# Kernel tuning notes

Measured on AMD Instinct MI355X. Metric: run time of the kernel, lower is better.

Reference implementation:

```python
import jax, jax.numpy as jnp
import numpy as np
import math
from functools import partial

B = 256
H = 256
HEADS = 4
DK = H // HEADS
NA_MAX, NP_MAX, NH_MAX = 127, 23, 11


def _counts():
    i = np.arange(B)
    ac = (64 + i % 64).astype(np.int32)   # atoms per graph, 64..127
    pc = (8 + i % 16).astype(np.int32)    # pharm fragments per graph, 8..23
    hc = (4 + i % 8).astype(np.int32)     # hyper-edges per graph, 4..11
    return ac, pc, hc


def setup_inputs() -> dict:
    key = jax.random.key(0)
    ks = jax.random.split(key, 32)
    ac, pc, hc = _counts()
    na, npm, nh = int(ac.sum()), int(pc.sum()), int(hc.sum())
    w = 1.0 / math.sqrt(H)
    inp = {
        'atom_message': jax.random.normal(ks[0], (na, H), jnp.float32),
        'pharm_message': jax.random.normal(ks[1], (npm, H), jnp.float32),
        'hyper_message': jax.random.normal(ks[2], (nh, H), jnp.float32),
        'atom_counts': jnp.asarray(ac),
        'pharm_counts': jnp.asarray(pc),
        'hyper_counts': jnp.asarray(hc),
    }
    # two MultiHeadedAttention blocks: q/k/v/out linears each (W stored as [in, out])
    names = []
    for pre in ('p2h', 'a2p'):
        for part in ('Wq', 'bq', 'Wk', 'bk', 'Wv', 'bv', 'Wo', 'bo'):
            names.append(f'{pre}_{part}')
    ki = 3
    for n in names:
        if n.split('_')[1].startswith('W'):
            inp[n] = jax.random.normal(ks[ki], (H, H), jnp.float32) * w
        else:
            inp[n] = jax.random.normal(ks[ki], (H,), jnp.float32) * 0.01
        ki += 1
    # bidirectional GRU params, torch layout: W_ih [3H, H], W_hh [3H, H], b [3H]
    for d in ('f', 'b'):
        inp[f'gru_Wih_{d}'] = jax.random.normal(ks[ki], (3 * H, H), jnp.float32) * w; ki += 1
        inp[f'gru_Whh_{d}'] = jax.random.normal(ks[ki], (3 * H, H), jnp.float32) * w; ki += 1
        inp[f'gru_bih_{d}'] = jax.random.normal(ks[ki], (3 * H,), jnp.float32) * 0.01; ki += 1
        inp[f'gru_bhh_{d}'] = jax.random.normal(ks[ki], (3 * H,), jnp.float32) * 0.01; ki += 1
    return inp


def _split_pad(msg, counts, max_n):
    # faithful vectorized version of split_batch: narrow + zero-pad per graph
    starts = jnp.concatenate([jnp.zeros((1,), jnp.int32), jnp.cumsum(counts)[:-1].astype(jnp.int32)])
    j = jnp.arange(max_n)
    valid = j[None, :] < counts[:, None]                       # [B, max_n]
    idx = jnp.where(valid, starts[:, None] + j[None, :], msg.shape[0])
    padded_src = jnp.concatenate([msg, jnp.zeros((1, msg.shape[1]), msg.dtype)], 0)
    return padded_src[idx], valid                              # [B, max_n, H]


def _mha(q, k, v, mask, Wq, bq, Wk, bk, Wv, bv, Wo, bo):
    Bq, Lq, _ = q.shape
    def proj(x, W, b):
        y = x @ W + b
        return y.reshape(x.shape[0], x.shape[1], HEADS, DK).transpose(0, 2, 1, 3)
    qh, kh, vh = proj(q, Wq, bq), proj(k, Wk, bk), proj(v, Wv, bv)
    scores = jnp.einsum('bhqd,bhkd->bhqk', qh, kh) / math.sqrt(DK)
    scores = jnp.where(mask[:, None], jnp.float32(-1e9), scores)
    p = jax.nn.softmax(scores, axis=-1)
    o = jnp.einsum('bhqk,bhkd->bhqd', p, vh)
    o = o.transpose(0, 2, 1, 3).reshape(Bq, Lq, H)
    return o @ Wo + bo


def _gru_dir(x, h0, Wih, Whh, bih, bhh):
    # x: [B, T, H], torch GRU cell equations
    def step(h, xt):
        gi = xt @ Wih.T + bih
        gh = h @ Whh.T + bhh
        ir, iz, inn = jnp.split(gi, 3, axis=-1)
        hr, hz, hn = jnp.split(gh, 3, axis=-1)
        r = jax.nn.sigmoid(ir + hr)
        z = jax.nn.sigmoid(iz + hz)
        n = jnp.tanh(inn + r * hn)
        h = (1.0 - z) * n + z * h
        return h, h
    _, ys = jax.lax.scan(step, h0, x.transpose(1, 0, 2))
    return ys.transpose(1, 0, 2)


def reference(atom_message, pharm_message, hyper_message,
              p2h_Wq, p2h_bq, p2h_Wk, p2h_bk, p2h_Wv, p2h_bv, p2h_Wo, p2h_bo,
              a2p_Wq, a2p_bq, a2p_Wk, a2p_bk, a2p_Wv, a2p_bv, a2p_Wo, a2p_bo,
              gru_Wih_f, gru_Whh_f, gru_bih_f, gru_bhh_f,
              gru_Wih_b, gru_Whh_b, gru_bih_b, gru_bhh_b,
              atom_counts, pharm_counts, hyper_counts):
    atom_f, atom_valid = _split_pad(atom_message, atom_counts, NA_MAX)
    pharm_f, _ = _split_pad(pharm_message, pharm_counts, NP_MAX)
    hyper_f, _ = _split_pad(hyper_message, hyper_counts, NH_MAX)

    nz = lambda t: (t != 0).astype(jnp.float32)
    mask1 = jnp.einsum('bqh,bkh->bqk', nz(pharm_f), nz(hyper_f)) == 0  # [B, Np, Nh]
    mask2 = jnp.einsum('bqh,bkh->bqk', nz(atom_f), nz(pharm_f)) == 0   # [B, Na, Np]

    pharm_f = _mha(pharm_f, hyper_f, hyper_f, mask1,
                   p2h_Wq, p2h_bq, p2h_Wk, p2h_bk, p2h_Wv, p2h_bv, p2h_Wo, p2h_bo) + pharm_f
    h = _mha(atom_f, pharm_f, pharm_f, mask2,
             a2p_Wq, a2p_bq, a2p_Wk, a2p_bk, a2p_Wv, a2p_bv, a2p_Wo, a2p_bo) + atom_f

    h0 = h.max(axis=1)  # initial hidden per direction
    hf = _gru_dir(h, h0, gru_Wih_f, gru_Whh_f, gru_bih_f, gru_bhh_f)
    hb = _gru_dir(h[:, ::-1], h0, gru_Wih_b, gru_Whh_b, gru_bih_b, gru_bhh_b)[:, ::-1]
    hcat = jnp.concatenate([hf, hb], axis=-1)  # [B, Na, 2H]

    v = atom_valid.astype(hcat.dtype)[..., None]
    graph_embed = (hcat * v).sum(axis=1) / atom_counts[:, None].astype(hcat.dtype)
    return graph_embed  # [B, 2H]
```

## Files before the change

### kernel.cpp

```cpp
#include <hip/hip_runtime.h>
#include <hip/hip_fp16.h>
#include <math.h>

#define NB 256
#define HDIM 256
#define NHEADS 4
#define DKH 64
#define LA 127
#define LP 23
#define LH 11

typedef _Float16 h2v __attribute__((ext_vector_type(2)));
typedef _Float16 f16x8 __attribute__((ext_vector_type(8)));
typedef float f32x4 __attribute__((ext_vector_type(4)));
union F4H { float4 f4; h2v h[4]; };

__device__ __forceinline__ float dot2acc(h2v a, h2v b, float c) {
#if __has_builtin(__builtin_amdgcn_fdot2)
  return __builtin_amdgcn_fdot2(a, b, c, false);
#else
  return c + (float)a[0] * (float)b[0] + (float)a[1] * (float)b[1];
#endif
}

__device__ __forceinline__ float sigm(float x) { return 1.0f / (1.0f + __expf(-x)); }
__device__ __forceinline__ float tanh_fast(float x) { return 2.0f / (1.0f + __expf(-2.0f * x)) - 1.0f; }

__global__ void k_scan(const int* __restrict__ ac, const int* __restrict__ pc,
                       const int* __restrict__ hc, int* __restrict__ sa,
                       int* __restrict__ sp, int* __restrict__ sh) {
  int t = threadIdx.x;
  if (t == 0) { int s = 0; for (int i = 0; i < NB; i++) { sa[i] = s; s += ac[i]; } }
  else if (t == 1) { int s = 0; for (int i = 0; i < NB; i++) { sp[i] = s; s += pc[i]; } }
  else if (t == 2) { int s = 0; for (int i = 0; i < NB; i++) { sh[i] = s; s += hc[i]; } }
}

__global__ void k_cvt16(const float* __restrict__ in, __half* __restrict__ out, int n) {
  int i = blockIdx.x * blockDim.x + threadIdx.x;
  if (i < n) out[i] = __float2half(in[i]);
}

__global__ void k_wprepT(const float* __restrict__ src, __half* __restrict__ dst, int N) {
  int d = blockIdx.x * blockDim.x + threadIdx.x;
  if (d >= N * 256) return;
  int u = d & 7;
  int lg = (d >> 3) & 3;
  int c = (d >> 5) % N;
  int k0b = (d >> 5) / N;
  dst[d] = __float2half(src[(size_t)c * 256 + k0b * 32 + lg * 8 + u]);
}

__global__ __launch_bounds__(256) void k_mfma_gi(
    const __half* __restrict__ A16, const __half* __restrict__ Wf,
    const float* __restrict__ bias, __half* __restrict__ Out, int N) {
  int w = threadIdx.x >> 6, l = threadIdx.x & 63;
  int row0 = blockIdx.x * 64 + w * 16;
  int col0 = blockIdx.y * 64;
  int lr = l & 15, lg = l >> 4;
  f32x4 acc[4] = {};
  const __half* arow = A16 + (size_t)(row0 + lr) * 256 + lg * 8;
#pragma unroll
  for (int k0b = 0; k0b < 8; k0b++) {
    f16x8 a = *(const f16x8*)(arow + k0b * 32);
#pragma unroll
    for (int nt = 0; nt < 4; nt++) {
      int c = col0 + nt * 16 + lr;
      f16x8 b = *(const f16x8*)(Wf + ((size_t)(k0b * N + c) * 4 + lg) * 8);
      acc[nt] = __builtin_amdgcn_mfma_f32_16x16x32_f16(a, b, acc[nt], 0, 0, 0);
    }
  }
#pragma unroll
  for (int nt = 0; nt < 4; nt++) {
    int c = col0 + nt * 16 + lr;
    float bv = bias[c];
#pragma unroll
    for (int r = 0; r < 4; r++) {
      int row = row0 + lg * 4 + r;
      Out[(size_t)row * N + c] = __float2half(acc[nt][r] + bv);
    }
  }
}

template <bool GATHER_A, bool RES_GATHER, bool OUT_HALF>
__global__ __launch_bounds__(256) void k_gemm(
    const float* __restrict__ A, const float* __restrict__ msg,
    const int* __restrict__ starts, const int* __restrict__ counts, int L,
    const float* __restrict__ W, const float* __restrict__ bias,
    const float* __restrict__ resmsg, float* __restrict__ C,
    __half* __restrict__ Ch, int N) {
  const int K = HDIM;
  __shared__ float As[16][76];
  __shared__ float Ws[16][72];
  int tid = threadIdx.x;
  int row0 = blockIdx.x * 64, col0 = blockIdx.y * 64;
  int arow = row0 + (tid >> 2);
  const float* asrc;
  if constexpr (GATHER_A) {
    int b = arow / L, t = arow - b * L;
    asrc = (t < counts[b]) ? (msg + (size_t)(starts[b] + t) * K) : nullptr;
  } else {
    asrc = A + (size_t)arow * K;
  }
  int ak = (tid & 3) * 4;
  int wk = tid >> 4, wn = (tid & 15) * 4;
  int ty = tid >> 4, tx = tid & 15;
  float acc[4][4] = {};
  for (int k0 = 0; k0 < K; k0 += 16) {
    float4 av = make_float4(0.f, 0.f, 0.f, 0.f);
    if (asrc) av = *(const float4*)(asrc + k0 + ak);
    float4 wv = *(const float4*)(W + (size_t)(k0 + wk) * N + col0 + wn);
    __syncthreads();
    int m = tid >> 2;
    As[ak + 0][m] = av.x; As[ak + 1][m] = av.y;
    As[ak + 2][m] = av.z; As[ak + 3][m] = av.w;
    *(float4*)&Ws[wk][wn] = wv;
    __syncthreads();
#pragma unroll
    for (int kk = 0; kk < 16; kk++) {
      float4 a = *(const float4*)&As[kk][ty * 4];
      float4 b = *(const float4*)&Ws[kk][tx * 4];
      acc[0][0] += a.x * b.x; acc[0][1] += a.x * b.y; acc[0][2] += a.x * b.z; acc[0][3] += a.x * b.w;
      acc[1][0] += a.y * b.x; acc[1][1] += a.y * b.y; acc[1][2] += a.y * b.z; acc[1][3] += a.y * b.w;
      acc[2][0] += a.z * b.x; acc[2][1] += a.z * b.y; acc[2][2] += a.z * b.z; acc[2][3] += a.z * b.w;
      acc[3][0] += a.w * b.x; acc[3][1] += a.w * b.y; acc[3][2] += a.w * b.z; acc[3][3] += a.w * b.w;
    }
  }
  float4 bv = *(const float4*)(bias + col0 + tx * 4);
#pragma unroll
  for (int i = 0; i < 4; i++) {
    int r = row0 + ty * 4 + i;
    float o0 = acc[i][0] + bv.x, o1 = acc[i][1] + bv.y,
          o2 = acc[i][2] + bv.z, o3 = acc[i][3] + bv.w;
    if constexpr (RES_GATHER) {
      int b = r / L, t = r - b * L;
      if (t < counts[b]) {
        float4 rv = *(const float4*)(resmsg + (size_t)(starts[b] + t) * K + col0 + tx * 4);
        o0 += rv.x; o1 += rv.y; o2 += rv.z; o3 += rv.w;
      }
    }
    size_t o = (size_t)r * N + col0 + tx * 4;
    if constexpr (OUT_HALF) {
      Ch[o] = __float2half(o0); Ch[o + 1] = __float2half(o1);
      Ch[o + 2] = __float2half(o2); Ch[o + 3] = __float2half(o3);
    } else {
      *(float4*)(C + o) = make_float4(o0, o1, o2, o3);
    }
  }
}

template <int LQ, int LK>
__global__ __launch_bounds__(128) void k_attn(
    float* __restrict__ q, const float* __restrict__ kbuf,
    const float* __restrict__ vbuf, const int* __restrict__ cq,
    const int* __restrict__ ck) {
  __shared__ float qs[LQ][65];
  __shared__ float ks[LK][65];
  __shared__ float vs[LK][65];
  int b = blockIdx.x, head = blockIdx.y;
  int tid = threadIdx.x;
  for (int idx = tid; idx < LQ * 16; idx += 128) {
    int i = idx >> 4, c = (idx & 15) * 4;
    float4 v = *(const float4*)(q + (size_t)(b * LQ + i) * HDIM + head * DKH + c);
    qs[i][c] = v.x; qs[i][c + 1] = v.y; qs[i][c + 2] = v.z; qs[i][c + 3] = v.w;
  }
  for (int idx = tid; idx < LK * 16; idx += 128) {
    int i = idx >> 4, c = (idx & 15) * 4;
    float4 v = *(const float4*)(kbuf + (size_t)(b * LK + i) * HDIM + head * DKH + c);
    ks[i][c] = v.x; ks[i][c + 1] = v.y; ks[i][c + 2] = v.z; ks[i][c + 3] = v.w;
    float4 w = *(const float4*)(vbuf + (size_t)(b * LK + i) * HDIM + head * DKH + c);
    vs[i][c] = w.x; vs[i][c + 1] = w.y; vs[i][c + 2] = w.z; vs[i][c + 3] = w.w;
  }
  __syncthreads();
  int nq = cq[b], nk = ck[b];
  for (int i = tid; i < LQ; i += 128) {
    float s[LK];
    float mx = -INFINITY;
    bool qv = i < nq;
#pragma unroll
    for (int k = 0; k < LK; k++) {
      float d = -1e9f;
      if (qv && k < nk) {
        float acc = 0.f;
        for (int c = 0; c < DKH; c++) acc += qs[i][c] * ks[k][c];
        d = acc * 0.125f;
      }
      s[k] = d;
      mx = fmaxf(mx, d);
    }
    float den = 0.f;
#pragma unroll
    for (int k = 0; k < LK; k++) { s[k] = expf(s[k] - mx); den += s[k]; }
    float inv = 1.0f / den;
    for (int c = 0; c < DKH; c++) {
      float acc = 0.f;
#pragma unroll
      for (int k = 0; k < LK; k++) acc += s[k] * vs[k][c];
      q[(size_t)(b * LQ + i) * HDIM + head * DKH + c] = acc * inv;
    }
  }
}

__global__ void k_rowmax(const float* __restrict__ h, float* __restrict__ h0) {
  int b = blockIdx.x, j = threadIdx.x;
  float m = -INFINITY;
  for (int t = 0; t < LA; t++) m = fmaxf(m, h[((size_t)b * LA + t) * HDIM + j]);
  h0[b * HDIM + j] = m;
}

__global__ __launch_bounds__(512, 2) void k_gru4(
    const float* __restrict__ h0, const __half* __restrict__ Wh_f,
    const __half* __restrict__ Wh_b, const __half* __restrict__ gi_f,
    const __half* __restrict__ gi_b, const float* __restrict__ bhh_f,
    const float* __restrict__ bhh_b, const int* __restrict__ ac,
    float* __restrict__ out) {
  int bid = blockIdx.x;
  int dir = bid & 1, pair = bid >> 1;
  int g0 = pair, g1 = pair + 128;
  int tid = threadIdx.x;
  int j = tid >> 1, half = tid & 1;
  const __half* W = dir ? Wh_b : Wh_f;
  const __half* gih = dir ? gi_b : gi_f;
  const float* bhh = dir ? bhh_b : bhh_f;

  F4H wr[16], wz[16], wn[16];
  {
    const float4* Wr4 = (const float4*)(W + (size_t)j * 256 + half * 128);
    const float4* Wz4 = (const float4*)(W + (size_t)(256 + j) * 256 + half * 128);
    const float4* Wn4 = (const float4*)(W + (size_t)(512 + j) * 256 + half * 128);
#pragma unroll
    for (int p = 0; p < 16; p++) wr[p].f4 = Wr4[p];
#pragma unroll
    for (int p = 0; p < 16; p++) wz[p].f4 = Wz4[p];
#pragma unroll
    for (int p = 0; p < 16; p++) wn[p].f4 = Wn4[p];
  }
  float br = bhh[j], bz = bhh[256 + j], bn = bhh[512 + j];
  int cnt = ac[g0];

  __shared__ __align__(16) __half hs[2][HDIM];
  float hprev0 = h0[(size_t)g0 * HDIM + j];
  float hprev1 = h0[(size_t)g1 * HDIM + j];
  if (half == 0) {
    hs[0][j] = __float2half(hprev0);
    hs[1][j] = __float2half(hprev1);
  }
  __syncthreads();

  const float4* h0p = (const float4*)hs[0] + half * 16;
  const float4* h1p = (const float4*)hs[1] + half * 16;
  float sum0 = 0.f, sum1 = 0.f;
  int nsteps = dir ? LA : cnt;
  for (int ti = 0; ti < nsteps; ti++) {
    int t = dir ? (LA - 1 - ti) : ti;
    const __half* gp0 = gih + ((size_t)g0 * LA + t) * 768 + j;
    const __half* gp1 = gih + ((size_t)g1 * LA + t) * 768 + j;
    float gr0 = __half2float(gp0[0]);
    float gz0 = __half2float(gp0[256]);
    float gn0 = __half2float(gp0[512]);
    float gr1 = __half2float(gp1[0]);
    float gz1 = __half2float(gp1[256]);
    float gn1 = __half2float(gp1[512]);
    float ap0 = 0.f, zp0 = 0.f, np0 = 0.f;
    float ap1 = 0.f, zp1 = 0.f, np1 = 0.f;
#pragma unroll
    for (int q = 0; q < 16; q++) {
      F4H hv0; hv0.f4 = h0p[q];
      F4H hv1; hv1.f4 = h1p[q];
#pragma unroll
      for (int u = 0; u < 4; u++) {
        ap0 = dot2acc(hv0.h[u], wr[q].h[u], ap0);
        zp0 = dot2acc(hv0.h[u], wz[q].h[u], zp0);
        np0 = dot2acc(hv0.h[u], wn[q].h[u], np0);
        ap1 = dot2acc(hv1.h[u], wr[q].h[u], ap1);
        zp1 = dot2acc(hv1.h[u], wz[q].h[u], zp1);
        np1 = dot2acc(hv1.h[u], wn[q].h[u], np1);
      }
    }
    ap0 += __shfl_xor(ap0, 1);
    zp0 += __shfl_xor(zp0, 1);
    np0 += __shfl_xor(np0, 1);
    ap1 += __shfl_xor(ap1, 1);
    zp1 += __shfl_xor(zp1, 1);
    np1 += __shfl_xor(np1, 1);
    float r0 = sigm(gr0 + br + ap0);
    float z0 = sigm(gz0 + bz + zp0);
    float n0 = tanh_fast(gn0 + bn + r0 * np0);
    float hnew0 = (1.f - z0) * n0 + z0 * hprev0;
    float r1 = sigm(gr1 + br + ap1);
    float z1 = sigm(gz1 + bz + zp1);
    float n1 = tanh_fast(gn1 + bn + r1 * np1);
    float hnew1 = (1.f - z1) * n1 + z1 * hprev1;
    __syncthreads();
    if (half == 0) {
      hs[0][j] = __float2half(hnew0);
      hs[1][j] = __float2half(hnew1);
    }
    hprev0 = hnew0;
    hprev1 = hnew1;
    if (t < cnt) { sum0 += hnew0; sum1 += hnew1; }
    __syncthreads();
  }
  if (half == 0) {
    out[(size_t)g0 * 512 + dir * 256 + j] = sum0 / (float)cnt;
    out[(size_t)g1 * 512 + dir * 256 + j] = sum1 / (float)cnt;
  }
}

extern "C" void kernel_launch(void* const* d_in, const int* in_sizes, int n_in,
                              void* d_out, int out_size, void* d_ws, size_t ws_size,
                              hipStream_t stream) {
  const float* atom_msg  = (const float*)d_in[0];
  const float* pharm_msg = (const float*)d_in[1];
  const float* hyper_msg = (const float*)d_in[2];
  const int* ac = (const int*)d_in[3];
  const int* pc = (const int*)d_in[4];
  const int* hc = (const int*)d_in[5];
  const float* p2h_Wq = (const float*)d_in[6];
  const float* p2h_bq = (const float*)d_in[7];
  const float* p2h_Wk = (const float*)d_in[8];
  const float* p2h_bk = (const float*)d_in[9];
  const float* p2h_Wv = (const float*)d_in[10];
  const float* p2h_bv = (const float*)d_in[11];
  const float* p2h_Wo = (const float*)d_in[12];
  const float* p2h_bo = (const float*)d_in[13];
  const float* a2p_Wq = (const float*)d_in[14];
  const float* a2p_bq = (const float*)d_in[15];
  const float* a2p_Wk = (const float*)d_in[16];
  const float* a2p_bk = (const float*)d_in[17];
  const float* a2p_Wv = (const float*)d_in[18];
  const float* a2p_bv = (const float*)d_in[19];
  const float* a2p_Wo = (const float*)d_in[20];
  const float* a2p_bo = (const float*)d_in[21];
  const float* Wih_f  = (const float*)d_in[22];
  const float* Whh_f  = (const float*)d_in[23];
  const float* bih_f  = (const float*)d_in[24];
  const float* bhh_f  = (const float*)d_in[25];
  const float* Wih_b  = (const float*)d_in[26];
  const float* Whh_b  = (const float*)d_in[27];
  const float* bih_b  = (const float*)d_in[28];
  const float* bhh_b  = (const float*)d_in[29];
  float* out = (float*)d_out;
  (void)in_sizes; (void)n_in; (void)out_size; (void)ws_size;

  char* wsb = (char*)d_ws;
  size_t off = 0;
  auto alloc = [&](size_t bytes) -> void* {
    void* p = wsb + off;
    off += (bytes + 255) & ~(size_t)255;
    return p;
  };
  int* sa = (int*)alloc(NB * 4);
  int* sp = (int*)alloc(NB * 4);
  int* sh = (int*)alloc(NB * 4);
  __half* Wh16_f = (__half*)alloc((size_t)768 * 256 * 2);
  __half* Wh16_b = (__half*)alloc((size_t)768 * 256 * 2);
  __half* Wf16_f = (__half*)alloc((size_t)768 * 256 * 2);
  __half* Wf16_b = (__half*)alloc((size_t)768 * 256 * 2);
  float* q_p = (float*)alloc((size_t)NB * LP * HDIM * 4);
  float* k_h = (float*)alloc((size_t)NB * LH * HDIM * 4);
  float* v_h = (float*)alloc((size_t)NB * LH * HDIM * 4);
  float* ph2 = (float*)alloc((size_t)NB * LP * HDIM * 4);
  float* q_a = (float*)alloc((size_t)NB * LA * HDIM * 4);
  float* k_p = (float*)alloc((size_t)NB * LP * HDIM * 4);
  float* v_p = (float*)alloc((size_t)NB * LP * HDIM * 4);
  float* h_x = (float*)alloc((size_t)NB * LA * HDIM * 4);
  __half* h_x16 = (__half*)alloc((size_t)NB * LA * HDIM * 2);
  float* h0  = (float*)alloc((size_t)NB * HDIM * 4);
  __half* gi_f = (__half*)alloc((size_t)NB * LA * 768 * 2);
  __half* gi_b = (__half*)alloc((size_t)NB * LA * 768 * 2);

  k_scan<<<1, 64, 0, stream>>>(ac, pc, hc, sa, sp, sh);
  int tb = (768 * 256 + 255) / 256;
  k_cvt16<<<tb, 256, 0, stream>>>(Whh_f, Wh16_f, 768 * 256);
  k_cvt16<<<tb, 256, 0, stream>>>(Whh_b, Wh16_b, 768 * 256);
  k_wprepT<<<tb, 256, 0, stream>>>(Wih_f, Wf16_f, 768);
  k_wprepT<<<tb, 256, 0, stream>>>(Wih_b, Wf16_b, 768);

  k_gemm<true, false, false><<<dim3(NB * LP / 64, 4), 256, 0, stream>>>(
      nullptr, pharm_msg, sp, pc, LP, p2h_Wq, p2h_bq, nullptr, q_p, nullptr, 256);
  k_gemm<true, false, false><<<dim3(NB * LH / 64, 4), 256, 0, stream>>>(
      nullptr, hyper_msg, sh, hc, LH, p2h_Wk, p2h_bk, nullptr, k_h, nullptr, 256);
  k_gemm<true, false, false><<<dim3(NB * LH / 64, 4), 256, 0, stream>>>(
      nullptr, hyper_msg, sh, hc, LH, p2h_Wv, p2h_bv, nullptr, v_h, nullptr, 256);
  k_attn<LP, LH><<<dim3(NB, NHEADS), 128, 0, stream>>>(q_p, k_h, v_h, pc, hc);
  k_gemm<false, true, false><<<dim3(NB * LP / 64, 4), 256, 0, stream>>>(
      q_p, nullptr, sp, pc, LP, p2h_Wo, p2h_bo, pharm_msg, ph2, nullptr, 256);

  k_gemm<true, false, false><<<dim3(NB * LA / 64, 4), 256, 0, stream>>>(
      nullptr, atom_msg, sa, ac, LA, a2p_Wq, a2p_bq, nullptr, q_a, nullptr, 256);
  k_gemm<false, false, false><<<dim3(NB * LP / 64, 4), 256, 0, stream>>>(
      ph2, nullptr, nullptr, nullptr, 1, a2p_Wk, a2p_bk, nullptr, k_p, nullptr, 256);
  k_gemm<false, false, false><<<dim3(NB * LP / 64, 4), 256, 0, stream>>>(
      ph2, nullptr, nullptr, nullptr, 1, a2p_Wv, a2p_bv, nullptr, v_p, nullptr, 256);
  k_attn<LA, LP><<<dim3(NB, NHEADS), 128, 0, stream>>>(q_a, k_p, v_p, ac, pc);
  k_gemm<false, true, false><<<dim3(NB * LA / 64, 4), 256, 0, stream>>>(
      q_a, nullptr, sa, ac, LA, a2p_Wo, a2p_bo, atom_msg, h_x, nullptr, 256);

  k_rowmax<<<NB, 256, 0, stream>>>(h_x, h0);
  k_cvt16<<<(NB * LA * HDIM + 255) / 256, 256, 0, stream>>>(h_x, h_x16, NB * LA * HDIM);
  k_mfma_gi<<<dim3(NB * LA / 64, 12), 256, 0, stream>>>(h_x16, Wf16_f, bih_f, gi_f, 768);
  k_mfma_gi<<<dim3(NB * LA / 64, 12), 256, 0, stream>>>(h_x16, Wf16_b, bih_b, gi_b, 768);
  k_gru4<<<NB, 512, 0, stream>>>(h0, Wh16_f, Wh16_b, gi_f, gi_b, bhh_f, bhh_b, ac, out);
}
```

Before: 805.0 us.

## Replace FP32 SIMT attention projection GEMMs with split-FP16 MFMA GEMMs

```diff
diff --git a/kernel.cpp b/kernel.cpp
--- a/kernel.cpp
+++ b/kernel.cpp
@@ -48,6 +48,89 @@
   int c = (d >> 5) % N;
   int k0b = (d >> 5) / N;
   dst[d] = __float2half(src[(size_t)c * 256 + k0b * 32 + lg * 8 + u]);
+}
+
+__global__ void k_wprep_pr(const float* __restrict__ src, __half* __restrict__ hi,
+                           __half* __restrict__ lo) {
+  int d = blockIdx.x * blockDim.x + threadIdx.x;
+  if (d >= 256 * 256) return;
+  int u = d & 7;
+  int lg = (d >> 3) & 3;
+  int c = (d >> 5) & 255;
+  int k0b = d >> 13;
+  float w = src[(size_t)(k0b * 32 + lg * 8 + u) * 256 + c];
+  __half h = __float2half(w);
+  hi[d] = h;
+  lo[d] = __float2half(w - __half2float(h));
+}
+
+__global__ void k_gsplit(const float* __restrict__ msg, const int* __restrict__ starts,
+                         const int* __restrict__ counts, int L, int M,
+                         __half* __restrict__ hi, __half* __restrict__ lo) {
+  int idx = blockIdx.x * blockDim.x + threadIdx.x;
+  if (idx >= M * 256) return;
+  int r = idx >> 8, c = idx & 255;
+  int b = r / L, t = r - b * L;
+  float v = (t < counts[b]) ? msg[(size_t)(starts[b] + t) * 256 + c] : 0.f;
+  __half h = __float2half(v);
+  hi[idx] = h;
+  lo[idx] = __float2half(v - __half2float(h));
+}
+
+__global__ void k_split(const float* __restrict__ in, int n,
+                        __half* __restrict__ hi, __half* __restrict__ lo) {
+  int idx = blockIdx.x * blockDim.x + threadIdx.x;
+  if (idx >= n) return;
+  float v = in[idx];
+  __half h = __float2half(v);
+  hi[idx] = h;
+  lo[idx] = __float2half(v - __half2float(h));
+}
+
+template <bool RES>
+__global__ __launch_bounds__(256) void k_mfma_sp(
+    const __half* __restrict__ Ahi, const __half* __restrict__ Alo,
+    const __half* __restrict__ Whi, const __half* __restrict__ Wlo,
+    const float* __restrict__ bias, const float* __restrict__ resmsg,
+    const int* __restrict__ starts, const int* __restrict__ counts, int L,
+    float* __restrict__ Out) {
+  int w = threadIdx.x >> 6, l = threadIdx.x & 63;
+  int row0 = blockIdx.x * 64 + w * 16;
+  int col0 = blockIdx.y * 64;
+  int lr = l & 15, lg = l >> 4;
+  f32x4 acc[4] = {};
+  const __half* ahrow = Ahi + (size_t)(row0 + lr) * 256 + lg * 8;
+  const __half* alrow = Alo + (size_t)(row0 + lr) * 256 + lg * 8;
+#pragma unroll
+  for (int k0b = 0; k0b < 8; k0b++) {
+    f16x8 ah = *(const f16x8*)(ahrow + k0b * 32);
+    f16x8 al = *(const f16x8*)(alrow + k0b * 32);
+#pragma unroll
+    for (int nt = 0; nt < 4; nt++) {
+      int c = col0 + nt * 16 + lr;
+      size_t wi = ((size_t)(k0b * 256 + c) * 4 + lg) * 8;
+      f16x8 bh = *(const f16x8*)(Whi + wi);
+      f16x8 bl = *(const f16x8*)(Wlo + wi);
+      acc[nt] = __builtin_amdgcn_mfma_f32_16x16x32_f16(ah, bh, acc[nt], 0, 0, 0);
+      acc[nt] = __builtin_amdgcn_mfma_f32_16x16x32_f16(al, bh, acc[nt], 0, 0, 0);
+      acc[nt] = __builtin_amdgcn_mfma_f32_16x16x32_f16(ah, bl, acc[nt], 0, 0, 0);
+    }
+  }
+#pragma unroll
+  for (int nt = 0; nt < 4; nt++) {
+    int c = col0 + nt * 16 + lr;
+    float bv = bias[c];
+#pragma unroll
+    for (int r = 0; r < 4; r++) {
+      int row = row0 + lg * 4 + r;
+      float o = acc[nt][r] + bv;
+      if constexpr (RES) {
+        int b = row / L, t = row - b * L;
+        if (t < counts[b]) o += resmsg[(size_t)(starts[b] + t) * 256 + c];
+      }
+      Out[(size_t)row * 256 + c] = o;
+    }
+  }
 }
 
 __global__ __launch_bounds__(256) void k_mfma_gi(
@@ -77,73 +160,6 @@
     for (int r = 0; r < 4; r++) {
       int row = row0 + lg * 4 + r;
       Out[(size_t)row * N + c] = __float2half(acc[nt][r] + bv);
-    }
-  }
-}
-
-template <bool GATHER_A, bool RES_GATHER, bool OUT_HALF>
-__global__ __launch_bounds__(256) void k_gemm(
-    const float* __restrict__ A, const float* __restrict__ msg,
-    const int* __restrict__ starts, const int* __restrict__ counts, int L,
-    const float* __restrict__ W, const float* __restrict__ bias,
-    const float* __restrict__ resmsg, float* __restrict__ C,
-    __half* __restrict__ Ch, int N) {
-  const int K = HDIM;
-  __shared__ float As[16][76];
-  __shared__ float Ws[16][72];
-  int tid = threadIdx.x;
-  int row0 = blockIdx.x * 64, col0 = blockIdx.y * 64;
-  int arow = row0 + (tid >> 2);
-  const float* asrc;
-  if constexpr (GATHER_A) {
-    int b = arow / L, t = arow - b * L;
-    asrc = (t < counts[b]) ? (msg + (size_t)(starts[b] + t) * K) : nullptr;
-  } else {
-    asrc = A + (size_t)arow * K;
-  }
-  int ak = (tid & 3) * 4;
-  int wk = tid >> 4, wn = (tid & 15) * 4;
-  int ty = tid >> 4, tx = tid & 15;
-  float acc[4][4] = {};
-  for (int k0 = 0; k0 < K; k0 += 16) {
-    float4 av = make_float4(0.f, 0.f, 0.f, 0.f);
-    if (asrc) av = *(const float4*)(asrc + k0 + ak);
-    float4 wv = *(const float4*)(W + (size_t)(k0 + wk) * N + col0 + wn);
-    __syncthreads();
-    int m = tid >> 2;
-    As[ak + 0][m] = av.x; As[ak + 1][m] = av.y;
-    As[ak + 2][m] = av.z; As[ak + 3][m] = av.w;
-    *(float4*)&Ws[wk][wn] = wv;
-    __syncthreads();
-#pragma unroll
-    for (int kk = 0; kk < 16; kk++) {
-      float4 a = *(const float4*)&As[kk][ty * 4];
-      float4 b = *(const float4*)&Ws[kk][tx * 4];
-      acc[0][0] += a.x * b.x; acc[0][1] += a.x * b.y; acc[0][2] += a.x * b.z; acc[0][3] += a.x * b.w;
-      acc[1][0] += a.y * b.x; acc[1][1] += a.y * b.y; acc[1][2] += a.y * b.z; acc[1][3] += a.y * b.w;
-      acc[2][0] += a.z * b.x; acc[2][1] += a.z * b.y; acc[2][2] += a.z * b.z; acc[2][3] += a.z * b.w;
-      acc[3][0] += a.w * b.x; acc[3][1] += a.w * b.y; acc[3][2] += a.w * b.z; acc[3][3] += a.w * b.w;
-    }
-  }
-  float4 bv = *(const float4*)(bias + col0 + tx * 4);
-#pragma unroll
-  for (int i = 0; i < 4; i++) {
-    int r = row0 + ty * 4 + i;
-    float o0 = acc[i][0] + bv.x, o1 = acc[i][1] + bv.y,
-          o2 = acc[i][2] + bv.z, o3 = acc[i][3] + bv.w;
-    if constexpr (RES_GATHER) {
-      int b = r / L, t = r - b * L;
-      if (t < counts[b]) {
-        float4 rv = *(const float4*)(resmsg + (size_t)(starts[b] + t) * K + col0 + tx * 4);
-        o0 += rv.x; o1 += rv.y; o2 += rv.z; o3 += rv.w;
-      }
-    }
-    size_t o = (size_t)r * N + col0 + tx * 4;
-    if constexpr (OUT_HALF) {
-      Ch[o] = __float2half(o0); Ch[o + 1] = __float2half(o1);
-      Ch[o + 2] = __float2half(o2); Ch[o + 3] = __float2half(o3);
-    } else {
-      *(float4*)(C + o) = make_float4(o0, o1, o2, o3);
     }
   }
 }
@@ -349,6 +365,7 @@
     off += (bytes + 255) & ~(size_t)255;
     return p;
   };
+  const int MA = NB * LA, MP = NB * LP, MH = NB * LH;
   int* sa = (int*)alloc(NB * 4);
   int* sp = (int*)alloc(NB * 4);
   int* sh = (int*)alloc(NB * 4);
@@ -356,18 +373,27 @@
   __half* Wh16_b = (__half*)alloc((size_t)768 * 256 * 2);
   __half* Wf16_f = (__half*)alloc((size_t)768 * 256 * 2);
   __half* Wf16_b = (__half*)alloc((size_t)768 * 256 * 2);
-  float* q_p = (float*)alloc((size_t)NB * LP * HDIM * 4);
-  float* k_h = (float*)alloc((size_t)NB * LH * HDIM * 4);
-  float* v_h = (float*)alloc((size_t)NB * LH * HDIM * 4);
-  float* ph2 = (float*)alloc((size_t)NB * LP * HDIM * 4);
-  float* q_a = (float*)alloc((size_t)NB * LA * HDIM * 4);
-  float* k_p = (float*)alloc((size_t)NB * LP * HDIM * 4);
-  float* v_p = (float*)alloc((size_t)NB * LP * HDIM * 4);
-  float* h_x = (float*)alloc((size_t)NB * LA * HDIM * 4);
-  __half* h_x16 = (__half*)alloc((size_t)NB * LA * HDIM * 2);
+  __half *Wp[8], *Wl[8];
+  for (int i = 0; i < 8; i++) {
+    Wp[i] = (__half*)alloc((size_t)256 * 256 * 2);
+    Wl[i] = (__half*)alloc((size_t)256 * 256 * 2);
+  }
+  float* q_p = (float*)alloc((size_t)MP * HDIM * 4);
+  float* k_h = (float*)alloc((size_t)MH * HDIM * 4);
+  float* v_h = (float*)alloc((size_t)MH * HDIM * 4);
+  float* ph2 = (float*)alloc((size_t)MP * HDIM * 4);
+  float* q_a = (float*)alloc((size_t)MA * HDIM * 4);
+  float* k_p = (float*)alloc((size_t)MP * HDIM * 4);
+  float* v_p = (float*)alloc((size_t)MP * HDIM * 4);
+  float* h_x = (float*)alloc((size_t)MA * HDIM * 4);
+  __half* h_x16 = (__half*)alloc((size_t)MA * HDIM * 2);
   float* h0  = (float*)alloc((size_t)NB * HDIM * 4);
-  __half* gi_f = (__half*)alloc((size_t)NB * LA * 768 * 2);
-  __half* gi_b = (__half*)alloc((size_t)NB * LA * 768 * 2);
+  __half* gi_f = (__half*)alloc((size_t)MA * 768 * 2);
+  __half* gi_b = (__half*)alloc((size_t)MA * 768 * 2);
+  __half* B1h = gi_b;
+  __half* B1l = gi_b + (size_t)MA * HDIM;
+  __half* B2h = gi_f;
+  __half* B2l = gi_f + (size_t)MA * HDIM;
 
   k_scan<<<1, 64, 0, stream>>>(ac, pc, hc, sa, sp, sh);
   int tb = (768 * 256 + 255) / 256;
@@ -375,30 +401,39 @@
   k_cvt16<<<tb, 256, 0, stream>>>(Whh_b, Wh16_b, 768 * 256);
   k_wprepT<<<tb, 256, 0, stream>>>(Wih_f, Wf16_f, 768);
   k_wprepT<<<tb, 256, 0, stream>>>(Wih_b, Wf16_b, 768);
-
-  k_gemm<true, false, false><<<dim3(NB * LP / 64, 4), 256, 0, stream>>>(
-      nullptr, pharm_msg, sp, pc, LP, p2h_Wq, p2h_bq, nullptr, q_p, nullptr, 256);
-  k_gemm<true, false, false><<<dim3(NB * LH / 64, 4), 256, 0, stream>>>(
-      nullptr, hyper_msg, sh, hc, LH, p2h_Wk, p2h_bk, nullptr, k_h, nullptr, 256);
-  k_gemm<true, false, false><<<dim3(NB * LH / 64, 4), 256, 0, stream>>>(
-      nullptr, hyper_msg, sh, hc, LH, p2h_Wv, p2h_bv, nullptr, v_h, nullptr, 256);
+  const float* pw[8] = {p2h_Wq, p2h_Wk, p2h_Wv, p2h_Wo, a2p_Wq, a2p_Wk, a2p_Wv, a2p_Wo};
+  for (int i = 0; i < 8; i++)
+    k_wprep_pr<<<256, 256, 0, stream>>>(pw[i], Wp[i], Wl[i]);
+
+  k_gsplit<<<(MP * 256 + 255) / 256, 256, 0, stream>>>(pharm_msg, sp, pc, LP, MP, B1h, B1l);
+  k_mfma_sp<false><<<dim3(MP / 64, 4), 256, 0, stream>>>(
+      B1h, B1l, Wp[0], Wl[0], p2h_bq, nullptr, nullptr, nullptr, 1, q_p);
+  k_gsplit<<<(MH * 256 + 255) / 256, 256, 0, stream>>>(hyper_msg, sh, hc, LH, MH, B2h, B2l);
+  k_mfma_sp<false><<<dim3(MH / 64, 4), 256, 0, stream>>>(
+      B2h, B2l, Wp[1], Wl[1], p2h_bk, nullptr, nullptr, nullptr, 1, k_h);
+  k_mfma_sp<false><<<dim3(MH / 64, 4), 256, 0, stream>>>(
+      B2h, B2l, Wp[2], Wl[2], p2h_bv, nullptr, nullptr, nullptr, 1, v_h);
   k_attn<LP, LH><<<dim3(NB, NHEADS), 128, 0, stream>>>(q_p, k_h, v_h, pc, hc);
-  k_gemm<false, true, false><<<dim3(NB * LP / 64, 4), 256, 0, stream>>>(
-      q_p, nullptr, sp, pc, LP, p2h_Wo, p2h_bo, pharm_msg, ph2, nullptr, 256);
-
-  k_gemm<true, false, false><<<dim3(NB * LA / 64, 4), 256, 0, stream>>>(
-      nullptr, atom_msg, sa, ac, LA, a2p_Wq, a2p_bq, nullptr, q_a, nullptr, 256);
-  k_gemm<false, false, false><<<dim3(NB * LP / 64, 4), 256, 0, stream>>>(
-      ph2, nullptr, nullptr, nullptr, 1, a2p_Wk, a2p_bk, nullptr, k_p, nullptr, 256);
-  k_gemm<false, false, false><<<dim3(NB * LP / 64, 4), 256, 0, stream>>>(
-      ph2, nullptr, nullptr, nullptr, 1, a2p_Wv, a2p_bv, nullptr, v_p, nullptr, 256);
+  k_split<<<(MP * 256 + 255) / 256, 256, 0, stream>>>(q_p, MP * 256, B1h, B1l);
+  k_mfma_sp<true><<<dim3(MP / 64, 4), 256, 0, stream>>>(
+      B1h, B1l, Wp[3], Wl[3], p2h_bo, pharm_msg, sp, pc, LP, ph2);
+
+  k_gsplit<<<(MA * 256 + 255) / 256, 256, 0, stream>>>(atom_msg, sa, ac, LA, MA, B2h, B2l);
+  k_mfma_sp<false><<<dim3(MA / 64, 4), 256, 0, stream>>>(
+      B2h, B2l, Wp[4], Wl[4], a2p_bq, nullptr, nullptr, nullptr, 1, q_a);
+  k_split<<<(MP * 256 + 255) / 256, 256, 0, stream>>>(ph2, MP * 256, B1h, B1l);
+  k_mfma_sp<false><<<dim3(MP / 64, 4), 256, 0, stream>>>(
+      B1h, B1l, Wp[5], Wl[5], a2p_bk, nullptr, nullptr, nullptr, 1, k_p);
+  k_mfma_sp<false><<<dim3(MP / 64, 4), 256, 0, stream>>>(
+      B1h, B1l, Wp[6], Wl[6], a2p_bv, nullptr, nullptr, nullptr, 1, v_p);
   k_attn<LA, LP><<<dim3(NB, NHEADS), 128, 0, stream>>>(q_a, k_p, v_p, ac, pc);
-  k_gemm<false, true, false><<<dim3(NB * LA / 64, 4), 256, 0, stream>>>(
-      q_a, nullptr, sa, ac, LA, a2p_Wo, a2p_bo, atom_msg, h_x, nullptr, 256);
+  k_split<<<(MA * 256 + 255) / 256, 256, 0, stream>>>(q_a, MA * 256, B2h, B2l);
+  k_mfma_sp<true><<<dim3(MA / 64, 4), 256, 0, stream>>>(
+      B2h, B2l, Wp[7], Wl[7], a2p_bo, atom_msg, sa, ac, LA, h_x);
 
   k_rowmax<<<NB, 256, 0, stream>>>(h_x, h0);
-  k_cvt16<<<(NB * LA * HDIM + 255) / 256, 256, 0, stream>>>(h_x, h_x16, NB * LA * HDIM);
-  k_mfma_gi<<<dim3(NB * LA / 64, 12), 256, 0, stream>>>(h_x16, Wf16_f, bih_f, gi_f, 768);
-  k_mfma_gi<<<dim3(NB * LA / 64, 12), 256, 0, stream>>>(h_x16, Wf16_b, bih_b, gi_b, 768);
+  k_cvt16<<<(MA * HDIM + 255) / 256, 256, 0, stream>>>(h_x, h_x16, MA * HDIM);
+  k_mfma_gi<<<dim3(MA / 64, 12), 256, 0, stream>>>(h_x16, Wf16_f, bih_f, gi_f, 768);
+  k_mfma_gi<<<dim3(MA / 64, 12), 256, 0, stream>>>(h_x16, Wf16_b, bih_b, gi_b, 768);
   k_gru4<<<NB, 512, 0, stream>>>(h0, Wh16_f, Wh16_b, gi_f, gi_b, bhh_f, bhh_b, ac, out);
 }
```

Measured after the change: 910.0 us. +13.0%, slower.
